# Kernel tuning notes

Measured on AMD Instinct MI355X. Metric: run time of the kernel, lower is better.

## Reference

```python
import jax, jax.numpy as jnp
import numpy as np

N, E = 50000, 800000
F_IN, F_OUT, H, F_EDGE = 256, 32, 8, 5
LEAKY_SLOPE = 0.2


def setup_inputs() -> dict:
    key = jax.random.key(0)
    ks = jax.random.split(key, 6)
    x = jax.random.normal(ks[0], (N, F_IN), dtype=jnp.float32)
    edge_index = jax.random.randint(ks[1], (2, E), 0, N, dtype=jnp.int64)
    edge_attr = jax.random.normal(ks[2], (E, F_EDGE), dtype=jnp.float32)
    degree_src = jax.random.randint(ks[3], (E,), 0, 64, dtype=jnp.int64)
    # Xavier-uniform params
    lim_W = float(np.sqrt(6.0 / (F_IN + F_OUT)))
    W = jax.random.uniform(ks[4], (H, F_IN, F_OUT), minval=-lim_W, maxval=lim_W, dtype=jnp.float32)
    A = 2 * F_OUT + F_EDGE
    lim_a = float(np.sqrt(6.0 / (H + A)))
    a = jax.random.uniform(ks[5], (H, A), minval=-lim_a, maxval=lim_a, dtype=jnp.float32)
    lim_e = float(np.sqrt(1.0 / F_EDGE))
    W_edge_w = jax.random.uniform(jax.random.fold_in(key, 7), (F_EDGE, F_EDGE), minval=-lim_e, maxval=lim_e, dtype=jnp.float32)
    return {"x": x, "edge_index": edge_index, "edge_attr": edge_attr,
            "degree_src": degree_src, "W": W, "a": a, "W_edge_w": W_edge_w}


def reference(x, edge_index, edge_attr, degree_src, W, a, W_edge_w):
    n = x.shape[0]
    h, f_out = W.shape[0], W.shape[2]
    src, dst = edge_index[0], edge_index[1]
    # per-head projection: (N, H, F_out)
    Wh = jnp.einsum('nf,hfo->nho', x, W)
    # split attention vector instead of materializing the concat
    a_src, a_dst, a_e = a[:, :f_out], a[:, f_out:2 * f_out], a[:, 2 * f_out:]
    ef = edge_attr @ W_edge_w.T                      # (E, F_edge)
    e = (jnp.einsum('eho,ho->eh', Wh[src], a_src)
         + jnp.einsum('eho,ho->eh', Wh[dst], a_dst)
         + ef @ a_e.T)                                # (E, H)
    e = jax.nn.leaky_relu(e, LEAKY_SLOPE)
    scale = 1.0 / jnp.sqrt(jnp.clip(degree_src.astype(jnp.float32), 1.0, None))
    e = e * scale[:, None]
    # segment softmax over src; torch scatter_reduce amax include_self=True with zeros init -> max includes 0
    e_max = jnp.maximum(jax.ops.segment_max(e, src, num_segments=n), 0.0)
    e_exp = jnp.exp(e - e_max[src])
    e_sum = jax.ops.segment_sum(e_exp, src, num_segments=n)
    alpha = e_exp / (e_sum[src] + 1e-16)             # (E, H)
    msg = Wh[dst] * alpha[:, :, None]                # (E, H, F_out)
    out = jax.ops.segment_sum(msg, src, num_segments=n)
    out = jax.nn.elu(out.reshape(n, h * f_out))
    return out, alpha
```

## Files before the change

### kernel.cpp

```cpp
#include <hip/hip_runtime.h>
#include <hip/hip_bf16.h>
#include <math.h>

#define NN 50000
#define NE 800000
#define FIN 256
#define FOUT 32
#define NH 8
#define FE 5
#define AROW 69
#define NROWS_PAD 50048

typedef float f32x4 __attribute__((ext_vector_type(4)));
typedef short bf16x8 __attribute__((ext_vector_type(8)));

static __device__ __forceinline__ unsigned short f2bf(float f) {
    unsigned u = __float_as_uint(f);
    unsigned r = (u + 0x7FFFu + ((u >> 16) & 1u)) >> 16;
    return (unsigned short)r;
}
static __device__ __forceinline__ float bf2f(unsigned short b) {
    return __uint_as_float(((unsigned)b) << 16);
}

__global__ __launch_bounds__(256) void k_prep(const float* __restrict__ W,
                                              const float* __restrict__ a,
                                              const float* __restrict__ Wew,
                                              float* __restrict__ C,
                                              unsigned short* __restrict__ Bh,
                                              unsigned short* __restrict__ Bl,
                                              unsigned short* __restrict__ Bsh,
                                              unsigned short* __restrict__ Bsl) {
    int t = threadIdx.x;
    if (blockIdx.x == 0) {
        if (t < NH * FE) {
            int h = t / FE, k = t % FE;
            float s = 0.f;
            for (int j = 0; j < FE; ++j) s += a[h * AROW + 2 * FOUT + j] * Wew[j * FE + k];
            C[t] = s;
        }
        int k = t;
        for (int h = 0; h < NH; ++h) {
            float s1v = 0.f, s2v = 0.f;
            for (int o = 0; o < FOUT; ++o) {
                float wv = W[(size_t)h * (FIN * FOUT) + (size_t)k * FOUT + o];
                s1v += wv * a[h * AROW + o];
                s2v += wv * a[h * AROW + FOUT + o];
            }
            unsigned short h1 = f2bf(s1v);
            Bsh[h * 256 + k] = h1;
            Bsl[h * 256 + k] = f2bf(s1v - bf2f(h1));
            unsigned short h2 = f2bf(s2v);
            Bsh[(8 + h) * 256 + k] = h2;
            Bsl[(8 + h) * 256 + k] = f2bf(s2v - bf2f(h2));
        }
    } else {
        int c = blockIdx.x - 1;
        int k = t;
        int h = c >> 5, o = c & 31;
        float f = W[(size_t)h * (FIN * FOUT) + (size_t)k * FOUT + o];
        unsigned short hi = f2bf(f);
        unsigned short lo = f2bf(f - bf2f(hi));
        Bh[c * 256 + k] = hi;
        Bl[c * 256 + k] = lo;
    }
}

__global__ __launch_bounds__(256) void k_pre2(const float* __restrict__ x,
                                              unsigned short* __restrict__ xb,
                                              const int* __restrict__ ei,
                                              int* __restrict__ counts,
                                              int* __restrict__ pos) {
    int i = blockIdx.x * 256 + threadIdx.x;
    if (i < (NN * FIN) / 8) {
        f32x4 u0 = *(const f32x4*)&x[(size_t)i * 8];
        f32x4 u1 = *(const f32x4*)&x[(size_t)i * 8 + 4];
        bf16x8 hi;
        hi[0] = (short)f2bf(u0.x); hi[1] = (short)f2bf(u0.y);
        hi[2] = (short)f2bf(u0.z); hi[3] = (short)f2bf(u0.w);
        hi[4] = (short)f2bf(u1.x); hi[5] = (short)f2bf(u1.y);
        hi[6] = (short)f2bf(u1.z); hi[7] = (short)f2bf(u1.w);
        *(bf16x8*)&xb[(size_t)i * 8] = hi;
    }
    if (i < NE / 4) {
        int4 e4 = *(const int4*)&ei[i * 4];
        int4 pv;
        pv.x = atomicAdd(&counts[e4.x], 1);
        pv.y = atomicAdd(&counts[e4.y], 1);
        pv.z = atomicAdd(&counts[e4.z], 1);
        pv.w = atomicAdd(&counts[e4.w], 1);
        *(int4*)&pos[i * 4] = pv;
    }
}

__global__ __launch_bounds__(256) void k_gemm_mfma(const unsigned short* __restrict__ xb,
                                                   const unsigned short* __restrict__ Bh,
                                                   const unsigned short* __restrict__ Bl,
                                                   const unsigned short* __restrict__ Bsh,
                                                   const unsigned short* __restrict__ Bsl,
                                                   unsigned short* __restrict__ Whb,
                                                   float* __restrict__ s1,
                                                   float* __restrict__ s2, int nrows) {
    int t = threadIdx.x;
    int w = t >> 6, l = t & 63;
    int r = l & 15, blk = l >> 4;
    int row0 = blockIdx.x * 64;
    int c0 = w * 64;

    f32x4 acc[4][4];
    f32x4 acc_s = (f32x4)(0.f);
#pragma unroll
    for (int i = 0; i < 4; ++i)
#pragma unroll
        for (int j = 0; j < 4; ++j) acc[i][j] = (f32x4)(0.f);

    const unsigned short* ap[4];
#pragma unroll
    for (int rt = 0; rt < 4; ++rt)
        ap[rt] = xb + (size_t)(row0 + rt * 16 + r) * 256 + blk * 8;

#pragma unroll
    for (int ks = 0; ks < 8; ++ks) {
        const int k0 = ks * 32;
        bf16x8 ah[4];
#pragma unroll
        for (int rt = 0; rt < 4; ++rt)
            ah[rt] = *(const bf16x8*)(ap[rt] + k0);
        bf16x8 bh[4], bl[4];
#pragma unroll
        for (int ct = 0; ct < 4; ++ct) {
            int c = c0 + ct * 16 + r;
            bh[ct] = *(const bf16x8*)&Bh[c * 256 + k0 + blk * 8];
            bl[ct] = *(const bf16x8*)&Bl[c * 256 + k0 + blk * 8];
        }
        bf16x8 bsh = *(const bf16x8*)&Bsh[r * 256 + k0 + blk * 8];
        bf16x8 bsl = *(const bf16x8*)&Bsl[r * 256 + k0 + blk * 8];
#pragma unroll
        for (int ct = 0; ct < 4; ++ct) {
#pragma unroll
            for (int rt = 0; rt < 4; ++rt) {
                acc[rt][ct] = __builtin_amdgcn_mfma_f32_16x16x32_bf16(ah[rt], bh[ct], acc[rt][ct], 0, 0, 0);
                acc[rt][ct] = __builtin_amdgcn_mfma_f32_16x16x32_bf16(ah[rt], bl[ct], acc[rt][ct], 0, 0, 0);
            }
        }
        acc_s = __builtin_amdgcn_mfma_f32_16x16x32_bf16(ah[w], bsh, acc_s, 0, 0, 0);
        acc_s = __builtin_amdgcn_mfma_f32_16x16x32_bf16(ah[w], bsl, acc_s, 0, 0, 0);
    }

#pragma unroll
    for (int rt = 0; rt < 4; ++rt) {
#pragma unroll
        for (int reg = 0; reg < 4; ++reg) {
            int row = row0 + rt * 16 + blk * 4 + reg;
            if (row < nrows) {
#pragma unroll
                for (int ct = 0; ct < 4; ++ct)
                    Whb[(size_t)row * 256 + c0 + ct * 16 + r] = f2bf(acc[rt][ct][reg]);
            }
        }
    }
#pragma unroll
    for (int reg = 0; reg < 4; ++reg) {
        int row = row0 + w * 16 + blk * 4 + reg;
        if (row < nrows) {
            if (r < 8) s1[row * NH + r] = acc_s[reg];
            else       s2[row * NH + (r - 8)] = acc_s[reg];
        }
    }
}

__global__ __launch_bounds__(256) void k_scanA(const int* __restrict__ counts,
                                               int* __restrict__ part,
                                               int* __restrict__ bsums, int n) {
    __shared__ int lds[256];
    int t = threadIdx.x;
    int base = blockIdx.x * 1024;
    int i0 = base + t * 4;
    int v0 = (i0 + 0 < n) ? counts[i0 + 0] : 0;
    int v1 = (i0 + 1 < n) ? counts[i0 + 1] : 0;
    int v2 = (i0 + 2 < n) ? counts[i0 + 2] : 0;
    int v3 = (i0 + 3 < n) ? counts[i0 + 3] : 0;
    int l0 = v0, l1 = l0 + v1, l2 = l1 + v2, l3 = l2 + v3;
    lds[t] = l3;
    __syncthreads();
    for (int off = 1; off < 256; off <<= 1) {
        int val = lds[t];
        if (t >= off) val += lds[t - off];
        __syncthreads();
        lds[t] = val;
        __syncthreads();
    }
    int excl = (t == 0) ? 0 : lds[t - 1];
    if (i0 + 0 < n) part[i0 + 0] = excl;
    if (i0 + 1 < n) part[i0 + 1] = excl + l0;
    if (i0 + 2 < n) part[i0 + 2] = excl + l1;
    if (i0 + 3 < n) part[i0 + 3] = excl + l2;
    if (t == 255) bsums[blockIdx.x] = lds[255];
}

__global__ void k_scanB(const int* __restrict__ bsums, int* __restrict__ boffs, int nb) {
    __shared__ int s[64];
    int t = threadIdx.x;
    int v = (t < nb) ? bsums[t] : 0;
    s[t] = v;
    __syncthreads();
    for (int off = 1; off < 64; off <<= 1) {
        int x = s[t];
        if (t >= off) x += s[t - off];
        __syncthreads();
        s[t] = x;
        __syncthreads();
    }
    if (t < nb) boffs[t] = s[t] - v;
}

__global__ __launch_bounds__(256) void k_scanC(int* __restrict__ row_ptr,
                                               const int* __restrict__ boffs, int n, int total) {
    int i = blockIdx.x * 256 + threadIdx.x;
    if (i < n) row_ptr[i] += boffs[i >> 10];
    else if (i == n) row_ptr[n] = total;
}

__global__ __launch_bounds__(256) void k_scatlog(const int* __restrict__ ei,
                                                 const float* __restrict__ eattr,
                                                 const int* __restrict__ degs,
                                                 const float* __restrict__ s1,
                                                 const float* __restrict__ s2,
                                                 const float* __restrict__ C,
                                                 const int* __restrict__ row_ptr,
                                                 const int* __restrict__ pos,
                                                 unsigned short* __restrict__ e_perm,
                                                 int2* __restrict__ de_perm) {
    __shared__ float Cl[NH * FE];
    int t = threadIdx.x;
    if (t < NH * FE) Cl[t] = C[t];
    __syncthreads();
    int e = blockIdx.x * 256 + t;
    if (e >= NE) return;
    int src = ei[e], dst = ei[NE + e];
    int dg = degs[e];
    float scale = rsqrtf((float)(dg > 1 ? dg : 1));
    float ea0 = eattr[(size_t)e * FE + 0];
    float ea1 = eattr[(size_t)e * FE + 1];
    float ea2 = eattr[(size_t)e * FE + 2];
    float ea3 = eattr[(size_t)e * FE + 3];
    float ea4 = eattr[(size_t)e * FE + 4];
    float4 s1a = *(const float4*)&s1[src * NH];
    float4 s1b = *(const float4*)&s1[src * NH + 4];
    float4 s2a = *(const float4*)&s2[dst * NH];
    float4 s2b = *(const float4*)&s2[dst * NH + 4];
    float vs1[8] = {s1a.x, s1a.y, s1a.z, s1a.w, s1b.x, s1b.y, s1b.z, s1b.w};
    float vs2[8] = {s2a.x, s2a.y, s2a.z, s2a.w, s2b.x, s2b.y, s2b.z, s2b.w};
    bf16x8 v;
#pragma unroll
    for (int h = 0; h < NH; ++h) {
        float q = vs1[h] + vs2[h] + ea0 * Cl[h * FE + 0] + ea1 * Cl[h * FE + 1] +
                  ea2 * Cl[h * FE + 2] + ea3 * Cl[h * FE + 3] + ea4 * Cl[h * FE + 4];
        q = q > 0.f ? q : 0.2f * q;
        v[h] = (short)f2bf(q * scale);
    }
    int p = row_ptr[src] + pos[e];
    *(bf16x8*)&e_perm[(size_t)p * 8] = v;
    de_perm[p] = make_int2(dst, e);
}

__global__ __launch_bounds__(256) void k_smmsg(const int* __restrict__ row_ptr,
                                               const unsigned short* __restrict__ e_perm,
                                               const int2* __restrict__ de_perm,
                                               const unsigned short* __restrict__ Whb,
                                               float* __restrict__ out_alpha,
                                               float* __restrict__ out) {
    __shared__ float al[4][256];
    __shared__ int dl[4][32];
    __shared__ int el[4][32];
    int t = threadIdx.x;
    int w = t >> 6, l = t & 63;
    int n = blockIdx.x * 4 + w;
    if (n >= NN) return;
    int start = row_ptr[n], deg = row_ptr[n + 1] - start;
    int j = l >> 3, h = l & 7;

    float vc[4];
#pragma unroll
    for (int q = 0; q < 4; ++q) {
        int b = j + 8 * q;
        vc[q] = (b < deg) ? bf2f(e_perm[(size_t)(start + b) * 8 + h]) : -1e30f;
    }
    float mx = 0.f;
#pragma unroll
    for (int q = 0; q < 4; ++q) mx = fmaxf(mx, vc[q]);
    for (int b = 32 + j; b < deg; b += 8)
        mx = fmaxf(mx, bf2f(e_perm[(size_t)(start + b) * 8 + h]));
    mx = fmaxf(mx, __shfl_xor(mx, 8));
    mx = fmaxf(mx, __shfl_xor(mx, 16));
    mx = fmaxf(mx, __shfl_xor(mx, 32));
    float m = mx;
    float ex[4];
    float sm = 0.f;
#pragma unroll
    for (int q = 0; q < 4; ++q) { ex[q] = __expf(vc[q] - m); sm += ex[q]; }
    for (int b = 32 + j; b < deg; b += 8)
        sm += __expf(bf2f(e_perm[(size_t)(start + b) * 8 + h]) - m);
    sm += __shfl_xor(sm, 8);
    sm += __shfl_xor(sm, 16);
    sm += __shfl_xor(sm, 32);
    float inv = 1.f / (sm + 1e-16f);
    f32x4 acc = (f32x4)(0.f);
    int hh = l >> 3;
    for (int base = 0; base < deg; base += 32) {
        int cnt = deg - base;
        if (cnt > 32) cnt = 32;
        if (l < cnt) {
            int2 de = de_perm[start + base + l];
            dl[w][l] = de.x;
            el[w][l] = de.y;
        }
        asm volatile("s_waitcnt lgkmcnt(0)" ::: "memory");
#pragma unroll
        for (int q = 0; q < 4; ++q) {
            int b = base + j + 8 * q;
            if (b < deg) {
                float av = (base == 0 ? ex[q]
                                      : __expf(bf2f(e_perm[(size_t)(start + b) * 8 + h]) - m)) * inv;
                al[w][(j + 8 * q) * 8 + h] = av;
                out_alpha[(size_t)el[w][j + 8 * q] * 8 + h] = av;
            }
        }
        asm volatile("s_waitcnt lgkmcnt(0)" ::: "memory");
        for (int jj = 0; jj < cnt; ++jj) {
            int d = dl[w][jj];
            float av = al[w][jj * 8 + hh];
            ushort4 u = *(const ushort4*)&Whb[(size_t)d * 256 + l * 4];
            acc.x += av * bf2f(u.x);
            acc.y += av * bf2f(u.y);
            acc.z += av * bf2f(u.z);
            acc.w += av * bf2f(u.w);
        }
        asm volatile("s_waitcnt lgkmcnt(0)" ::: "memory");
    }
    f32x4 o;
    o.x = acc.x > 0.f ? acc.x : expm1f(acc.x);
    o.y = acc.y > 0.f ? acc.y : expm1f(acc.y);
    o.z = acc.z > 0.f ? acc.z : expm1f(acc.z);
    o.w = acc.w > 0.f ? acc.w : expm1f(acc.w);
    *(f32x4*)&out[(size_t)n * 256 + l * 4] = o;
}

extern "C" void kernel_launch(void* const* d_in, const int* in_sizes, int n_in,
                              void* d_out, int out_size, void* d_ws, size_t ws_size,
                              hipStream_t stream) {
    const float* x     = (const float*)d_in[0];
    const int*   ei    = (const int*)d_in[1];
    const float* eattr = (const float*)d_in[2];
    const int*   degs  = (const int*)d_in[3];
    const float* W     = (const float*)d_in[4];
    const float* a     = (const float*)d_in[5];
    const float* Wew   = (const float*)d_in[6];

    float* out       = (float*)d_out;
    float* out_alpha = out + (size_t)NN * 256;

    char* p = (char*)d_ws;
    auto alloc = [&](size_t bytes) -> char* {
        char* r = p;
        p += (bytes + 255) & ~(size_t)255;
        return r;
    };
    unsigned short* Whb     = (unsigned short*)alloc((size_t)NN * 256 * 2);
    unsigned short* xb      = (unsigned short*)alloc((size_t)NROWS_PAD * 256 * 2);
    float*          s1      = (float*)alloc((size_t)NN * NH * 4);
    float*          s2      = (float*)alloc((size_t)NN * NH * 4);
    float*          Cm      = (float*)alloc(NH * FE * 4);
    unsigned short* Bh      = (unsigned short*)alloc((size_t)256 * 256 * 2);
    unsigned short* Bl      = (unsigned short*)alloc((size_t)256 * 256 * 2);
    unsigned short* Bsh     = (unsigned short*)alloc((size_t)16 * 256 * 2);
    unsigned short* Bsl     = (unsigned short*)alloc((size_t)16 * 256 * 2);
    int*            counts  = (int*)alloc((size_t)NN * 4);
    int*            row_ptr = (int*)alloc((size_t)(NN + 1) * 4);
    int*            bsums   = (int*)alloc(64 * 4);
    int*            boffs   = (int*)alloc(64 * 4);
    int*            pos     = (int*)alloc((size_t)NE * 4);
    unsigned short* e_perm  = (unsigned short*)alloc((size_t)NE * NH * 2);
    int2*           de_perm = (int2*)alloc((size_t)NE * 8);

    hipMemsetAsync(counts, 0, (size_t)NN * 4, stream);

    k_prep<<<257, 256, 0, stream>>>(W, a, Wew, Cm, Bh, Bl, Bsh, Bsl);
    k_pre2<<<(NN * FIN / 8 + 255) / 256, 256, 0, stream>>>(x, xb, ei, counts, pos);
    k_gemm_mfma<<<(NN + 63) / 64, 256, 0, stream>>>(xb, Bh, Bl, Bsh, Bsl, Whb, s1, s2, NN);
    k_scanA<<<(NN + 1023) / 1024, 256, 0, stream>>>(counts, row_ptr, bsums, NN);
    k_scanB<<<1, 64, 0, stream>>>(bsums, boffs, (NN + 1023) / 1024);
    k_scanC<<<(NN + 1 + 255) / 256, 256, 0, stream>>>(row_ptr, boffs, NN, NE);
    k_scatlog<<<(NE + 255) / 256, 256, 0, stream>>>(ei, eattr, degs, s1, s2, Cm,
                                                    row_ptr, pos, e_perm, de_perm);
    k_smmsg<<<(NN + 3) / 4, 256, 0, stream>>>(row_ptr, e_perm, de_perm, Whb,
                                              out_alpha, out);
}
```

Before: 254.9 us.

## Write alpha in edge order via separate kernel using per-node max and inverse sum

The scattered per-element alpha writes inside the softmax/message kernel are removed. Instead, the logits are also stored in original edge order, the per-node max and inverse sum are saved, and a new edge-parallel kernel recomputes alpha with coalesced vector stores. This removes the uncoalesced 4-byte scatter writes and the edge-id gather. In exchange it adds an extra launch, an extra 12.8MB logit write and read, and a gather of per-source stats.

```diff
diff --git a/kernel.cpp b/kernel.cpp
--- a/kernel.cpp
+++ b/kernel.cpp
@@ -230,7 +230,8 @@
                                                  const int* __restrict__ row_ptr,
                                                  const int* __restrict__ pos,
                                                  unsigned short* __restrict__ e_perm,
-                                                 int2* __restrict__ de_perm) {
+                                                 unsigned short* __restrict__ e_orig,
+                                                 int* __restrict__ d_perm) {
     __shared__ float Cl[NH * FE];
     int t = threadIdx.x;
     if (t < NH * FE) Cl[t] = C[t];
@@ -261,18 +262,18 @@
     }
     int p = row_ptr[src] + pos[e];
     *(bf16x8*)&e_perm[(size_t)p * 8] = v;
-    de_perm[p] = make_int2(dst, e);
+    *(bf16x8*)&e_orig[(size_t)e * 8] = v;
+    d_perm[p] = dst;
 }
 
 __global__ __launch_bounds__(256) void k_smmsg(const int* __restrict__ row_ptr,
                                                const unsigned short* __restrict__ e_perm,
-                                               const int2* __restrict__ de_perm,
+                                               const int* __restrict__ d_perm,
                                                const unsigned short* __restrict__ Whb,
-                                               float* __restrict__ out_alpha,
+                                               float* __restrict__ minv,
                                                float* __restrict__ out) {
     __shared__ float al[4][256];
     __shared__ int dl[4][32];
-    __shared__ int el[4][32];
     int t = threadIdx.x;
     int w = t >> 6, l = t & 63;
     int n = blockIdx.x * 4 + w;
@@ -305,16 +306,16 @@
     sm += __shfl_xor(sm, 16);
     sm += __shfl_xor(sm, 32);
     float inv = 1.f / (sm + 1e-16f);
+    if (l < 8) {
+        minv[(size_t)n * 16 + l] = m;
+        minv[(size_t)n * 16 + 8 + l] = inv;
+    }
     f32x4 acc = (f32x4)(0.f);
     int hh = l >> 3;
     for (int base = 0; base < deg; base += 32) {
         int cnt = deg - base;
         if (cnt > 32) cnt = 32;
-        if (l < cnt) {
-            int2 de = de_perm[start + base + l];
-            dl[w][l] = de.x;
-            el[w][l] = de.y;
-        }
+        if (l < cnt) dl[w][l] = d_perm[start + base + l];
         asm volatile("s_waitcnt lgkmcnt(0)" ::: "memory");
 #pragma unroll
         for (int q = 0; q < 4; ++q) {
@@ -323,7 +324,6 @@
                 float av = (base == 0 ? ex[q]
                                       : __expf(bf2f(e_perm[(size_t)(start + b) * 8 + h]) - m)) * inv;
                 al[w][(j + 8 * q) * 8 + h] = av;
-                out_alpha[(size_t)el[w][j + 8 * q] * 8 + h] = av;
             }
         }
         asm volatile("s_waitcnt lgkmcnt(0)" ::: "memory");
@@ -344,6 +344,31 @@
     o.z = acc.z > 0.f ? acc.z : expm1f(acc.z);
     o.w = acc.w > 0.f ? acc.w : expm1f(acc.w);
     *(f32x4*)&out[(size_t)n * 256 + l * 4] = o;
+}
+
+__global__ __launch_bounds__(256) void k_alpha(const int* __restrict__ ei,
+                                               const unsigned short* __restrict__ e_orig,
+                                               const float* __restrict__ minv,
+                                               float* __restrict__ out_alpha) {
+    int e = blockIdx.x * 256 + threadIdx.x;
+    if (e >= NE) return;
+    int src = ei[e];
+    bf16x8 lv = *(const bf16x8*)&e_orig[(size_t)e * 8];
+    f32x4 m0 = *(const f32x4*)&minv[(size_t)src * 16];
+    f32x4 m1 = *(const f32x4*)&minv[(size_t)src * 16 + 4];
+    f32x4 i0 = *(const f32x4*)&minv[(size_t)src * 16 + 8];
+    f32x4 i1 = *(const f32x4*)&minv[(size_t)src * 16 + 12];
+    f32x4 o0, o1;
+    o0.x = __expf(bf2f(lv[0]) - m0.x) * i0.x;
+    o0.y = __expf(bf2f(lv[1]) - m0.y) * i0.y;
+    o0.z = __expf(bf2f(lv[2]) - m0.z) * i0.z;
+    o0.w = __expf(bf2f(lv[3]) - m0.w) * i0.w;
+    o1.x = __expf(bf2f(lv[4]) - m1.x) * i1.x;
+    o1.y = __expf(bf2f(lv[5]) - m1.y) * i1.y;
+    o1.z = __expf(bf2f(lv[6]) - m1.z) * i1.z;
+    o1.w = __expf(bf2f(lv[7]) - m1.w) * i1.w;
+    *(f32x4*)&out_alpha[(size_t)e * 8] = o0;
+    *(f32x4*)&out_alpha[(size_t)e * 8 + 4] = o1;
 }
 
 extern "C" void kernel_launch(void* const* d_in, const int* in_sizes, int n_in,
@@ -381,7 +406,9 @@
     int*            boffs   = (int*)alloc(64 * 4);
     int*            pos     = (int*)alloc((size_t)NE * 4);
     unsigned short* e_perm  = (unsigned short*)alloc((size_t)NE * NH * 2);
-    int2*           de_perm = (int2*)alloc((size_t)NE * 8);
+    unsigned short* e_orig  = (unsigned short*)alloc((size_t)NE * NH * 2);
+    int*            d_perm  = (int*)alloc((size_t)NE * 4);
+    float*          minv    = (float*)alloc((size_t)NN * 16 * 4);
 
     hipMemsetAsync(counts, 0, (size_t)NN * 4, stream);
 
@@ -392,7 +419,7 @@
     k_scanB<<<1, 64, 0, stream>>>(bsums, boffs, (NN + 1023) / 1024);
     k_scanC<<<(NN + 1 + 255) / 256, 256, 0, stream>>>(row_ptr, boffs, NN, NE);
     k_scatlog<<<(NE + 255) / 256, 256, 0, stream>>>(ei, eattr, degs, s1, s2, Cm,
-                                                    row_ptr, pos, e_perm, de_perm);
-    k_smmsg<<<(NN + 3) / 4, 256, 0, stream>>>(row_ptr, e_perm, de_perm, Whb,
-                                              out_alpha, out);
-}
+                                                    row_ptr, pos, e_perm, e_orig, d_perm);
+    k_smmsg<<<(NN + 3) / 4, 256, 0, stream>>>(row_ptr, e_perm, d_perm, Whb, minv, out);
+    k_alpha<<<(NE + 255) / 256, 256, 0, stream>>>(ei, e_orig, minv, out_alpha);
+}
```

Measured after the change: 269.4 us. +5.7%, slower.
